# Kernel tuning notes

Hardware: AMD Instinct MI355X
Metric: run time of the kernel (lower is better)

## Reference

```python
import jax, jax.numpy as jnp
import numpy as np

N_NODES = 100000
NEG_SLOPE = 0.2  # PyG GATConv default LeakyReLU slope


def gat_conv(x, W, att_src, att_dst, bias, edge_index, num_nodes, concat):
    """PyG-style GATConv with default add_self_loops=True.
    x: [N, Fin], W: [Fin, H*C], att_src/att_dst: [H, C], bias: [H*C] or [C].
    """
    H, C = att_src.shape
    h = (x @ W).reshape(num_nodes, H, C)              # [N, H, C]
    # append self-loops (PyG default)
    loops = jnp.arange(num_nodes, dtype=edge_index.dtype)
    src = jnp.concatenate([edge_index[0], loops])     # [E+N]
    dst = jnp.concatenate([edge_index[1], loops])
    # per-node attention logits, then per-edge score
    a_src = jnp.sum(h * att_src[None], axis=-1)       # [N, H]
    a_dst = jnp.sum(h * att_dst[None], axis=-1)       # [N, H]
    e = jax.nn.leaky_relu(a_src[src] + a_dst[dst], NEG_SLOPE)  # [E+N, H]
    # softmax over incoming edges of each destination node
    m = jax.ops.segment_max(e, dst, num_segments=num_nodes)    # [N, H]
    e = jnp.exp(e - m[dst])
    denom = jax.ops.segment_sum(e, dst, num_segments=num_nodes)
    alpha = e / denom[dst]                                      # [E+N, H]
    # scatter-aggregate weighted source features
    msg = h[src] * alpha[..., None]                             # [E+N, H, C]
    out = jax.ops.segment_sum(msg, dst, num_segments=num_nodes)  # [N, H, C]
    if concat:
        out = out.reshape(num_nodes, H * C)
    else:
        out = out.mean(axis=1)
    return out + bias


def setup_inputs() -> dict:
    key = jax.random.key(0)
    ks = jax.random.split(key, 12)
    N, E = N_NODES, 1600000
    Fin, Ch, Hh, Cout = 128, 64, 2, 64

    def glorot(k, shape):
        fan = shape[0] + shape[-1]
        return jax.random.uniform(k, shape, jnp.float32, -1.0, 1.0) * np.sqrt(6.0 / fan)

    x = jax.random.normal(ks[0], (N, Fin), jnp.float32)
    edge_index = jax.random.randint(ks[1], (2, E), 0, N, jnp.int32)
    W1 = glorot(ks[2], (Fin, Hh * Ch))
    att_src1 = glorot(ks[3], (Hh, Ch))
    att_dst1 = glorot(ks[4], (Hh, Ch))
    b1 = jnp.zeros((Hh * Ch,), jnp.float32)
    W2 = glorot(ks[5], (Hh * Ch, Cout))
    att_src2 = glorot(ks[6], (1, Cout))
    att_dst2 = glorot(ks[7], (1, Cout))
    b2 = jnp.zeros((Cout,), jnp.float32)
    return {"x": x, "edge_index": edge_index,
            "W1": W1, "att_src1": att_src1, "att_dst1": att_dst1, "b1": b1,
            "W2": W2, "att_src2": att_src2, "att_dst2": att_dst2, "b2": b2}


def reference(x, edge_index, W1, att_src1, att_dst1, b1, W2, att_src2, att_dst2, b2):
    h = gat_conv(x, W1, att_src1, att_dst1, b1, edge_index, N_NODES, concat=True)
    h = jax.nn.elu(h)
    out = gat_conv(h, W2, att_src2, att_dst2, b2, edge_index, N_NODES, concat=True)
    return out
```

## Files before the change

kernel.cpp:

```cpp
#include <hip/hip_runtime.h>
#include <hip/hip_bf16.h>
#include <cstdint>
#include <cstddef>

static constexpr int FIN = 128;
static constexpr int HC1 = 128;
static constexpr int EPB = 4096;

typedef __attribute__((ext_vector_type(8))) short short8;
typedef __attribute__((ext_vector_type(4))) float f32x4;

__device__ __forceinline__ float bf2f(unsigned int u) { return __uint_as_float(u << 16); }
__device__ __forceinline__ unsigned short f2bf(float f) {
  unsigned int u = __float_as_uint(f);
  return (unsigned short)((u + 0x7fff + ((u >> 16) & 1)) >> 16);
}
__device__ __forceinline__ float lrelu02(float x) { return x > 0.f ? x : 0.2f * x; }
__device__ __forceinline__ int rl_i(int v, int l) { return __builtin_amdgcn_readlane(v, l); }
__device__ __forceinline__ unsigned int q8b(float x, float inv) {
  float q = fminf(fmaxf(x * inv, -127.f), 127.f);
  return (unsigned int)((int)rintf(q) + 128) & 255u;
}
#define NEG_INF __int_as_float(0xff800000)

__global__ __launch_bounds__(256) void bucket_hist(const int* __restrict__ dst,
                                                   int* __restrict__ bhist, int E, int NB) {
  __shared__ int lh[512];
  int t = threadIdx.x;
  lh[t] = 0; lh[t + 256] = 0;
  __syncthreads();
  int e0 = blockIdx.x * EPB;
  #pragma unroll
  for (int i = 0; i < EPB / 256; i++) {
    int e = e0 + i * 256 + t;
    if (e < E) atomicAdd(&lh[dst[e] >> 8], 1);
  }
  __syncthreads();
  for (int x = t; x < NB; x += 256) {
    int c = lh[x];
    if (c > 0) atomicAdd(&bhist[x], c);
  }
}

__global__ __launch_bounds__(512) void scan_buckets(const int* __restrict__ bhist,
                                                    int* __restrict__ boffs, int n) {
  __shared__ int sh[512];
  int t = threadIdx.x;
  int v = (t < n) ? bhist[t] : 0;
  sh[t] = v; __syncthreads();
  for (int d = 1; d < 512; d <<= 1) {
    int w = (t >= d) ? sh[t - d] : 0;
    __syncthreads();
    sh[t] += w;
    __syncthreads();
  }
  if (t <= n) boffs[t] = sh[t] - v;
}

__global__ __launch_bounds__(256) void bucket_scatter(const int* __restrict__ src,
                                                      const int* __restrict__ dst,
                                                      const int* __restrict__ boffs,
                                                      int* __restrict__ gcur,
                                                      unsigned int* __restrict__ sorted,
                                                      int E, int NB) {
  __shared__ int lh[512];
  int t = threadIdx.x;
  lh[t] = 0; lh[t + 256] = 0;
  __syncthreads();
  int e0 = blockIdx.x * EPB;
  #pragma unroll
  for (int i = 0; i < EPB / 256; i++) {
    int e = e0 + i * 256 + t;
    if (e < E) atomicAdd(&lh[dst[e] >> 8], 1);
  }
  __syncthreads();
  for (int x = t; x < NB; x += 256) {
    int c = lh[x];
    lh[x] = (c > 0) ? (boffs[x] + atomicAdd(&gcur[x], c)) : 0;
  }
  __syncthreads();
  #pragma unroll
  for (int i = 0; i < EPB / 256; i++) {
    int e = e0 + i * 256 + t;
    if (e < E) {
      int d = dst[e];
      int pos = atomicAdd(&lh[d >> 8], 1);
      sorted[pos] = ((unsigned int)src[e] << 8) | (unsigned int)(d & 255);
    }
  }
}

__global__ __launch_bounds__(256) void bucket_place_fused(const unsigned int* __restrict__ sorted,
                                                          const int* __restrict__ boffs,
                                                          int* __restrict__ offs,
                                                          int* __restrict__ ssrc,
                                                          int N, int E) {
  __shared__ int cnt[256];
  __shared__ int pref[256];
  int b = blockIdx.x, t = threadIdx.x;
  cnt[t] = 0;
  __syncthreads();
  int beg = boffs[b], end = boffs[b + 1];
  for (int p = beg + t; p < end; p += 256)
    atomicAdd(&cnt[sorted[p] & 255u], 1);
  __syncthreads();
  int v = cnt[t];
  pref[t] = v; __syncthreads();
  for (int d = 1; d < 256; d <<= 1) {
    int w = (t >= d) ? pref[t - d] : 0;
    __syncthreads();
    pref[t] += w;
    __syncthreads();
  }
  int excl = pref[t] - v;
  int node = b * 256 + t;
  if (node < N) offs[node] = beg + excl;
  if (b == 0 && t == 0) offs[N] = E;
  cnt[t] = beg + excl;
  __syncthreads();
  for (int p = beg + t; p < end; p += 256) {
    unsigned int pk = sorted[p];
    int dl = pk & 255u;
    int r = atomicAdd(&cnt[dl], 1);
    ssrc[r] = (int)(pk >> 8);
  }
}

template <int COLS, bool AF32>
__global__ __launch_bounds__(256) void gemm_mfma(const void* __restrict__ Av,
                                                 const float* __restrict__ Wv,
                                                 const float* __restrict__ att_s,
                                                 const float* __restrict__ att_d,
                                                 unsigned char* __restrict__ Cq,
                                                 float* __restrict__ scl,
                                                 float* __restrict__ asrc,
                                                 float* __restrict__ adst,
                                                 int nrows) {
  constexpr int NT = COLS / 16;
  constexpr int H = COLS / 64;
  __shared__ unsigned short WT[COLS][136];
  __shared__ __align__(16) unsigned char pack[4][16 * COLS];

  const int tid = threadIdx.x;
  constexpr int NPC = COLS / 4;
  for (int idx = tid; idx < 128 * NPC; idx += 256) {
    int k = idx / NPC;
    int n0 = (idx - k * NPC) * 4;
    float4 wv = *(const float4*)(Wv + (size_t)k * COLS + n0);
    WT[n0 + 0][k] = f2bf(wv.x);
    WT[n0 + 1][k] = f2bf(wv.y);
    WT[n0 + 2][k] = f2bf(wv.z);
    WT[n0 + 3][k] = f2bf(wv.w);
  }

  const int w = tid >> 6, lane = tid & 63;
  const int quad = lane >> 4, cl = lane & 15;
  const int rbase = blockIdx.x * 128 + w * 32;

  float asv[NT], adv[NT];
  #pragma unroll
  for (int ct = 0; ct < NT; ct++) {
    asv[ct] = att_s[ct * 16 + cl];
    adv[ct] = att_d[ct * 16 + cl];
  }
  __syncthreads();

  f32x4 acc[2][NT];
  #pragma unroll
  for (int rt = 0; rt < 2; rt++)
    #pragma unroll
    for (int ct = 0; ct < NT; ct++) acc[rt][ct] = (f32x4){0.f, 0.f, 0.f, 0.f};

  #pragma unroll
  for (int kc = 0; kc < 4; kc++) {
    const int k0 = kc * 32 + quad * 8;
    short8 a[2];
    #pragma unroll
    for (int rt = 0; rt < 2; rt++) {
      int row = rbase + rt * 16 + cl;
      row = min(row, nrows - 1);
      if constexpr (AF32) {
        const float* ap = (const float*)Av + (size_t)row * 128 + k0;
        float4 f0 = *(const float4*)ap;
        float4 f1 = *(const float4*)(ap + 4);
        short8 t;
        t[0] = (short)f2bf(f0.x); t[1] = (short)f2bf(f0.y);
        t[2] = (short)f2bf(f0.z); t[3] = (short)f2bf(f0.w);
        t[4] = (short)f2bf(f1.x); t[5] = (short)f2bf(f1.y);
        t[6] = (short)f2bf(f1.z); t[7] = (short)f2bf(f1.w);
        a[rt] = t;
      } else {
        a[rt] = *(const short8*)((const unsigned short*)Av + (size_t)row * 128 + k0);
      }
    }
    #pragma unroll
    for (int ct = 0; ct < NT; ct++) {
      short8 b = *(const short8*)&WT[ct * 16 + cl][k0];
      #pragma unroll
      for (int rt = 0; rt < 2; rt++)
        acc[rt][ct] = __builtin_amdgcn_mfma_f32_16x16x32_bf16(a[rt], b, acc[rt][ct], 0, 0, 0);
    }
  }

  #pragma unroll
  for (int rt = 0; rt < 2; rt++) {
    #pragma unroll
    for (int r = 0; r < 4; r++) {
      int grow = rbase + rt * 16 + quad * 4 + r;
      float s0 = 0.f, s1 = 0.f, d0 = 0.f, d1 = 0.f;
      float mx = 0.f;
      #pragma unroll
      for (int ct = 0; ct < NT; ct++) {
        float av = acc[rt][ct][r];
        mx = fmaxf(mx, fabsf(av));
        if (H == 2 && ct >= NT / 2) {
          s1 = fmaf(av, asv[ct], s1);
          d1 = fmaf(av, adv[ct], d1);
        } else {
          s0 = fmaf(av, asv[ct], s0);
          d0 = fmaf(av, adv[ct], d0);
        }
      }
      #pragma unroll
      for (int dd = 8; dd >= 1; dd >>= 1) {
        mx = fmaxf(mx, __shfl_xor(mx, dd));
        s0 += __shfl_xor(s0, dd);
        d0 += __shfl_xor(d0, dd);
        if (H == 2) {
          s1 += __shfl_xor(s1, dd);
          d1 += __shfl_xor(d1, dd);
        }
      }
      float inv = mx > 0.f ? 127.f / mx : 0.f;
      if (cl == 0 && grow < nrows) {
        scl[grow] = mx * (1.f / 127.f);
        if (H == 2) {
          ((float2*)asrc)[grow] = make_float2(s0, s1);
          ((float2*)adst)[grow] = make_float2(d0, d1);
        } else {
          asrc[grow] = s0;
          adst[grow] = d0;
        }
      }
      #pragma unroll
      for (int ct = 0; ct < NT; ct++)
        pack[w][(quad * 4 + r) * COLS + ct * 16 + cl] =
            (unsigned char)q8b(acc[rt][ct][r], inv);
    }
    __syncthreads();
    if constexpr (COLS == 128) {
      #pragma unroll
      for (int i = 0; i < 2; i++) {
        int off = i * 1024 + lane * 16;
        uint4 v = *(const uint4*)&pack[w][off];
        int grow = rbase + rt * 16 + (off >> 7);
        if (grow < nrows)
          *(uint4*)(Cq + (size_t)grow * 128 + (off & 127)) = v;
      }
    } else {
      int off = lane * 16;
      uint4 v = *(const uint4*)&pack[w][off];
      int grow = rbase + rt * 16 + (off >> 6);
      if (grow < nrows)
        *(uint4*)(Cq + (size_t)grow * 64 + (off & 63)) = v;
    }
    __syncthreads();
  }
}

template <int H, bool ELU_OUT, bool F32OUT>
__global__ __launch_bounds__(256) void agg_gather(const void* __restrict__ hq,
                                                  const float* __restrict__ scl,
                                                  const float* __restrict__ asrc,
                                                  const float* __restrict__ adst,
                                                  const int* __restrict__ offs,
                                                  const int* __restrict__ ssrc,
                                                  const float* __restrict__ bias,
                                                  void* __restrict__ outv, int n) {
  __shared__ float pshare[4][64];
  __shared__ int vshare[4][64];
  const int tid = threadIdx.x;
  const int wid = tid >> 6;
  int node = (int)((blockIdx.x * (unsigned)blockDim.x + tid) >> 6);
  int lane = tid & 63;
  if (node >= n) return;
  const int hd = lane >> 5;
  const int beg = offs[node], end = offs[node + 1];
  const unsigned short* hq16 = (const unsigned short*)hq;
  const unsigned char* hqb = (const unsigned char*)hq;

  float adh, p_self, acc0, acc1;
  const float s_self = scl[node];
  if constexpr (H == 2) {
    float2 adv = ((const float2*)adst)[node];
    float2 asv = ((const float2*)asrc)[node];
    adh = hd ? adv.y : adv.x;
    p_self = __expf(lrelu02((hd ? asv.y : asv.x) + adh));
    unsigned int v = hq16[((size_t)node << 6) + lane];
    float ps = p_self * s_self;
    acc0 = ps * ((float)(v & 255u) - 128.f);
    acc1 = ps * ((float)((v >> 8) & 255u) - 128.f);
  } else {
    adh = adst[node];
    p_self = __expf(lrelu02(asrc[node] + adh));
    if (hd == 0) {
      unsigned int v = hq16[((size_t)node << 5) + lane];
      float ps = p_self * s_self;
      acc0 = ps * ((float)(v & 255u) - 128.f);
      acc1 = ps * ((float)((v >> 8) & 255u) - 128.f);
    } else {
      acc0 = 0.f; acc1 = 0.f;
    }
  }
  float dacc = 0.f;
  float SPF = 0.f;

  constexpr int CH = (H == 2) ? 32 : 64;
  const int lvoff = (lane & 31) * 2;
  for (int pos = beg; pos < end; pos += CH) {
    const int len = min(CH, end - pos);
    int li = (H == 2) ? (lane & 31) : lane;
    bool valid = li < len;
    int s_l = valid ? ssrc[pos + li] : 0;
    float scl_l = valid ? scl[s_l] : 0.f;
    float a;
    if constexpr (H == 2) a = asrc[(s_l << 1) + hd];
    else                  a = asrc[s_l];
    float e_l = lrelu02(a + adh);
    float p_l = valid ? __expf(e_l) : 0.f;
    dacc += p_l;
    p_l *= scl_l;
    SPF += p_l;
    pshare[wid][lane] = p_l;
    if constexpr (H == 1) vshare[wid][lane] = s_l << 6;

    if constexpr (H == 2) {
      const int ng = (len + 7) >> 3;
      for (int g = 0; g < ng; g++) {
        const int jb = g * 8;
        unsigned short v[8];
        #pragma unroll
        for (int k = 0; k < 8; k++) {
          int s = rl_i(s_l, jb + k);
          v[k] = hq16[((size_t)(unsigned)s << 6) + lane];
        }
        float pv[8];
        #pragma unroll
        for (int k = 0; k < 8; k++) pv[k] = pshare[wid][hd * 32 + jb + k];
        #pragma unroll
        for (int k = 0; k < 8; k++) {
          unsigned int w = v[k];
          acc0 = fmaf(pv[k], (float)(w & 255u), acc0);
          acc1 = fmaf(pv[k], (float)((w >> 8) & 255u), acc1);
        }
      }
    } else {
      const int npair = (len + 1) >> 1;
      const int ng = (npair + 7) >> 3;
      for (int g = 0; g < ng; g++) {
        const int jb = g * 16;
        unsigned short v[8];
        #pragma unroll
        for (int k = 0; k < 8; k++) {
          int voff = vshare[wid][jb + 2 * k + hd];
          v[k] = *(const unsigned short*)(hqb + (unsigned)voff + lvoff);
        }
        float pv[8];
        #pragma unroll
        for (int k = 0; k < 8; k++) pv[k] = pshare[wid][jb + 2 * k + hd];
        #pragma unroll
        for (int k = 0; k < 8; k++) {
          unsigned int w = v[k];
          acc0 = fmaf(pv[k], (float)(w & 255u), acc0);
          acc1 = fmaf(pv[k], (float)((w >> 8) & 255u), acc1);
        }
      }
    }
  }

  if constexpr (H == 2) {
    #pragma unroll
    for (int dlt = 16; dlt >= 1; dlt >>= 1) {
      dacc += __shfl_xor(dacc, dlt);
      SPF  += __shfl_xor(SPF, dlt);
    }
  } else {
    #pragma unroll
    for (int dlt = 32; dlt >= 1; dlt >>= 1) {
      dacc += __shfl_xor(dacc, dlt);
      SPF  += __shfl_xor(SPF, dlt);
    }
    acc0 += __shfl_xor(acc0, 32);
    acc1 += __shfl_xor(acc1, 32);
  }
  acc0 = fmaf(-128.f, SPF, acc0);
  acc1 = fmaf(-128.f, SPF, acc1);
  const float d = p_self + dacc;

  const float inv = 1.f / d;
  if constexpr (H == 2) {
    float2 bv = ((const float2*)bias)[lane];
    float v0 = acc0 * inv + bv.x;
    float v1 = acc1 * inv + bv.y;
    if (ELU_OUT) {
      v0 = v0 > 0.f ? v0 : (__expf(v0) - 1.f);
      v1 = v1 > 0.f ? v1 : (__expf(v1) - 1.f);
    }
    if constexpr (F32OUT) {
      ((float2*)outv)[(size_t)node * 64 + lane] = make_float2(v0, v1);
    } else {
      unsigned int pk = (unsigned int)f2bf(v0) | ((unsigned int)f2bf(v1) << 16);
      ((unsigned int*)outv)[(size_t)node * 64 + lane] = pk;
    }
  } else {
    if (hd == 0) {
      float2 bv = ((const float2*)bias)[lane];
      float v0 = acc0 * inv + bv.x;
      float v1 = acc1 * inv + bv.y;
      if (ELU_OUT) {
        v0 = v0 > 0.f ? v0 : (__expf(v0) - 1.f);
        v1 = v1 > 0.f ? v1 : (__expf(v1) - 1.f);
      }
      if constexpr (F32OUT) {
        ((float2*)outv)[(size_t)node * 32 + lane] = make_float2(v0, v1);
      } else {
        unsigned int pk = (unsigned int)f2bf(v0) | ((unsigned int)f2bf(v1) << 16);
        ((unsigned int*)outv)[(size_t)node * 32 + lane] = pk;
      }
    }
  }
}

extern "C" void kernel_launch(void* const* d_in, const int* in_sizes, int n_in,
                              void* d_out, int out_size, void* d_ws, size_t ws_size,
                              hipStream_t stream) {
  const int N = in_sizes[0] / FIN;
  const int E = in_sizes[1] / 2;

  const void*  x   = d_in[0];
  const int*   ei  = (const int*)d_in[1];
  const float* W1  = (const float*)d_in[2];
  const float* as1 = (const float*)d_in[3];
  const float* ad1 = (const float*)d_in[4];
  const float* b1  = (const float*)d_in[5];
  const float* W2  = (const float*)d_in[6];
  const float* as2 = (const float*)d_in[7];
  const float* ad2 = (const float*)d_in[8];
  const float* b2  = (const float*)d_in[9];

  const int* e_src = ei;
  const int* e_dst = ei + E;

  char* p = (char*)d_ws;
  auto carve = [&](size_t bytes) {
    char* q = p;
    p += (bytes + 255) & ~(size_t)255;
    return (void*)q;
  };
  unsigned char* h1q = (unsigned char*)carve((size_t)N * 128);
  float* scl1        = (float*)carve((size_t)N * 4);
  unsigned char* h2q = (unsigned char*)carve((size_t)N * 64);
  float* scl2        = (float*)carve((size_t)N * 4);
  unsigned short* buf2 = (unsigned short*)carve((size_t)N * HC1 * 2);
  float* asrc1 = (float*)carve((size_t)N * 2 * 4);
  float* adst1 = (float*)carve((size_t)N * 2 * 4);
  float* asrc2 = (float*)carve((size_t)N * 4);
  float* adst2 = (float*)carve((size_t)N * 4);
  int* offs    = (int*)carve((size_t)(N + 1) * 4);
  int* bhist   = (int*)carve((size_t)2 * 512 * 4);
  int* gcur    = bhist + 512;
  int* boffs   = (int*)carve(513 * 4);
  unsigned int* sorted = (unsigned int*)carve((size_t)E * 4);
  int* ssrc    = (int*)carve((size_t)E * 4);

  const int NB = (N + 255) >> 8;
  const int sgrid = (E + EPB - 1) / EPB;
  const int wgrid = (int)(((size_t)N * 64 + 255) / 256);
  const int ggrid = (N + 127) / 128;

  hipMemsetAsync(bhist, 0, (size_t)2 * 512 * 4, stream);
  bucket_hist<<<sgrid, 256, 0, stream>>>(e_dst, bhist, E, NB);
  scan_buckets<<<1, 512, 0, stream>>>(bhist, boffs, NB);
  bucket_scatter<<<sgrid, 256, 0, stream>>>(e_src, e_dst, boffs, gcur, sorted, E, NB);
  bucket_place_fused<<<NB, 256, 0, stream>>>(sorted, boffs, offs, ssrc, N, E);

  gemm_mfma<128, true><<<ggrid, 256, 0, stream>>>(x, W1, as1, ad1, h1q, scl1,
                                                  asrc1, adst1, N);
  agg_gather<2, true, false><<<wgrid, 256, 0, stream>>>(h1q, scl1, asrc1, adst1,
                                                        offs, ssrc, b1, buf2, N);

  gemm_mfma<64, false><<<ggrid, 256, 0, stream>>>(buf2, W2, as2, ad2, h2q, scl2,
                                                  asrc2, adst2, N);
  agg_gather<1, false, true><<<wgrid, 256, 0, stream>>>(h2q, scl2, asrc2, adst2,
                                                        offs, ssrc, b2, d_out, N);
}
```

Before: 306.3 us.

## Store node features as fp16 and aggregate with packed fdot2 online softmax

Replaces the per-row int8 quantized node features (with per-node scale) with fp16 storage, doubling the gather bytes per edge but removing the scale loads and dequantization arithmetic. The aggregation switches to an online max-subtracted softmax and uses packed fp16 probabilities with v_dot2 instructions to accumulate two edges per instruction. It trades memory traffic in the gather-heavy aggregation for fewer ALU ops and better numerical accuracy.

```diff
diff --git a/kernel.cpp b/kernel.cpp
--- a/kernel.cpp
+++ b/kernel.cpp
@@ -9,17 +9,22 @@
 
 typedef __attribute__((ext_vector_type(8))) short short8;
 typedef __attribute__((ext_vector_type(4))) float f32x4;
-
-__device__ __forceinline__ float bf2f(unsigned int u) { return __uint_as_float(u << 16); }
+typedef __attribute__((ext_vector_type(2))) _Float16 f16x2;
+typedef decltype(__builtin_amdgcn_cvt_pkrtz(0.f, 0.f)) pk16x2;
+
 __device__ __forceinline__ unsigned short f2bf(float f) {
   unsigned int u = __float_as_uint(f);
   return (unsigned short)((u + 0x7fff + ((u >> 16) & 1)) >> 16);
 }
+__device__ __forceinline__ unsigned short f2h(float f) {
+  union { _Float16 h; unsigned short u; } c; c.h = (_Float16)f; return c.u;
+}
 __device__ __forceinline__ float lrelu02(float x) { return x > 0.f ? x : 0.2f * x; }
 __device__ __forceinline__ int rl_i(int v, int l) { return __builtin_amdgcn_readlane(v, l); }
-__device__ __forceinline__ unsigned int q8b(float x, float inv) {
-  float q = fminf(fmaxf(x * inv, -127.f), 127.f);
-  return (unsigned int)((int)rintf(q) + 128) & 255u;
+__device__ __forceinline__ float fdot2u(unsigned int a, unsigned int b, float c) {
+  union { unsigned int u; f16x2 h; } ua, ub;
+  ua.u = a; ub.u = b;
+  return __builtin_amdgcn_fdot2(ua.h, ub.h, c, false);
 }
 #define NEG_INF __int_as_float(0xff800000)
 
@@ -132,14 +137,13 @@
                                                  const float* __restrict__ att_s,
                                                  const float* __restrict__ att_d,
                                                  unsigned char* __restrict__ Cq,
-                                                 float* __restrict__ scl,
                                                  float* __restrict__ asrc,
                                                  float* __restrict__ adst,
                                                  int nrows) {
   constexpr int NT = COLS / 16;
   constexpr int H = COLS / 64;
   __shared__ unsigned short WT[COLS][136];
-  __shared__ __align__(16) unsigned char pack[4][16 * COLS];
+  __shared__ __align__(16) unsigned short pack16[4][16 * COLS];
 
   const int tid = threadIdx.x;
   constexpr int NPC = COLS / 4;
@@ -208,11 +212,9 @@
     for (int r = 0; r < 4; r++) {
       int grow = rbase + rt * 16 + quad * 4 + r;
       float s0 = 0.f, s1 = 0.f, d0 = 0.f, d1 = 0.f;
-      float mx = 0.f;
       #pragma unroll
       for (int ct = 0; ct < NT; ct++) {
         float av = acc[rt][ct][r];
-        mx = fmaxf(mx, fabsf(av));
         if (H == 2 && ct >= NT / 2) {
           s1 = fmaf(av, asv[ct], s1);
           d1 = fmaf(av, adv[ct], d1);
@@ -223,7 +225,6 @@
       }
       #pragma unroll
       for (int dd = 8; dd >= 1; dd >>= 1) {
-        mx = fmaxf(mx, __shfl_xor(mx, dd));
         s0 += __shfl_xor(s0, dd);
         d0 += __shfl_xor(d0, dd);
         if (H == 2) {
@@ -231,9 +232,7 @@
           d1 += __shfl_xor(d1, dd);
         }
       }
-      float inv = mx > 0.f ? 127.f / mx : 0.f;
       if (cl == 0 && grow < nrows) {
-        scl[grow] = mx * (1.f / 127.f);
         if (H == 2) {
           ((float2*)asrc)[grow] = make_float2(s0, s1);
           ((float2*)adst)[grow] = make_float2(d0, d1);
@@ -244,25 +243,27 @@
       }
       #pragma unroll
       for (int ct = 0; ct < NT; ct++)
-        pack[w][(quad * 4 + r) * COLS + ct * 16 + cl] =
-            (unsigned char)q8b(acc[rt][ct][r], inv);
+        pack16[w][(quad * 4 + r) * COLS + ct * 16 + cl] = f2h(acc[rt][ct][r]);
     }
     __syncthreads();
     if constexpr (COLS == 128) {
+      #pragma unroll
+      for (int i = 0; i < 4; i++) {
+        int off = i * 1024 + lane * 16;
+        uint4 v = *(const uint4*)((const char*)pack16[w] + off);
+        int grow = rbase + rt * 16 + (off >> 8);
+        if (grow < nrows)
+          *(uint4*)(Cq + (size_t)grow * 256 + (off & 255)) = v;
+      }
+    } else {
       #pragma unroll
       for (int i = 0; i < 2; i++) {
         int off = i * 1024 + lane * 16;
-        uint4 v = *(const uint4*)&pack[w][off];
+        uint4 v = *(const uint4*)((const char*)pack16[w] + off);
         int grow = rbase + rt * 16 + (off >> 7);
         if (grow < nrows)
           *(uint4*)(Cq + (size_t)grow * 128 + (off & 127)) = v;
       }
-    } else {
-      int off = lane * 16;
-      uint4 v = *(const uint4*)&pack[w][off];
-      int grow = rbase + rt * 16 + (off >> 6);
-      if (grow < nrows)
-        *(uint4*)(Cq + (size_t)grow * 64 + (off & 63)) = v;
     }
     __syncthreads();
   }
@@ -270,15 +271,13 @@
 
 template <int H, bool ELU_OUT, bool F32OUT>
 __global__ __launch_bounds__(256) void agg_gather(const void* __restrict__ hq,
-                                                  const float* __restrict__ scl,
                                                   const float* __restrict__ asrc,
                                                   const float* __restrict__ adst,
                                                   const int* __restrict__ offs,
                                                   const int* __restrict__ ssrc,
                                                   const float* __restrict__ bias,
                                                   void* __restrict__ outv, int n) {
-  __shared__ float pshare[4][64];
-  __shared__ int vshare[4][64];
+  __shared__ unsigned int pshare[4][32];
   const int tid = threadIdx.x;
   const int wid = tid >> 6;
   int node = (int)((blockIdx.x * (unsigned)blockDim.x + tid) >> 6);
@@ -286,118 +285,103 @@
   if (node >= n) return;
   const int hd = lane >> 5;
   const int beg = offs[node], end = offs[node + 1];
+  const unsigned int* hq32 = (const unsigned int*)hq;
   const unsigned short* hq16 = (const unsigned short*)hq;
-  const unsigned char* hqb = (const unsigned char*)hq;
-
-  float adh, p_self, acc0, acc1;
-  const float s_self = scl[node];
+
+  float adh, m, acc0, acc1;
   if constexpr (H == 2) {
     float2 adv = ((const float2*)adst)[node];
     float2 asv = ((const float2*)asrc)[node];
     adh = hd ? adv.y : adv.x;
-    p_self = __expf(lrelu02((hd ? asv.y : asv.x) + adh));
-    unsigned int v = hq16[((size_t)node << 6) + lane];
-    float ps = p_self * s_self;
-    acc0 = ps * ((float)(v & 255u) - 128.f);
-    acc1 = ps * ((float)((v >> 8) & 255u) - 128.f);
+    m = lrelu02((hd ? asv.y : asv.x) + adh);
+    union { unsigned int u; f16x2 h; } c;
+    c.u = hq32[((size_t)node << 6) + lane];
+    acc0 = (float)c.h[0];
+    acc1 = (float)c.h[1];
   } else {
     adh = adst[node];
-    p_self = __expf(lrelu02(asrc[node] + adh));
-    if (hd == 0) {
-      unsigned int v = hq16[((size_t)node << 5) + lane];
-      float ps = p_self * s_self;
-      acc0 = ps * ((float)(v & 255u) - 128.f);
-      acc1 = ps * ((float)((v >> 8) & 255u) - 128.f);
-    } else {
-      acc0 = 0.f; acc1 = 0.f;
-    }
-  }
+    m = lrelu02(asrc[node] + adh);
+    union { unsigned short u; _Float16 h; } c;
+    c.u = hq16[((size_t)node << 6) + lane];
+    acc0 = (float)c.h;
+    acc1 = 0.f;
+  }
+  float dsf = 1.f;
   float dacc = 0.f;
-  float SPF = 0.f;
 
   constexpr int CH = (H == 2) ? 32 : 64;
-  const int lvoff = (lane & 31) * 2;
   for (int pos = beg; pos < end; pos += CH) {
     const int len = min(CH, end - pos);
     int li = (H == 2) ? (lane & 31) : lane;
     bool valid = li < len;
     int s_l = valid ? ssrc[pos + li] : 0;
-    float scl_l = valid ? scl[s_l] : 0.f;
     float a;
     if constexpr (H == 2) a = asrc[(s_l << 1) + hd];
     else                  a = asrc[s_l];
-    float e_l = lrelu02(a + adh);
-    float p_l = valid ? __expf(e_l) : 0.f;
-    dacc += p_l;
-    p_l *= scl_l;
-    SPF += p_l;
-    pshare[wid][lane] = p_l;
-    if constexpr (H == 1) vshare[wid][lane] = s_l << 6;
+    float e_l = valid ? lrelu02(a + adh) : NEG_INF;
+    float mc = e_l;
+    #pragma unroll
+    for (int dlt = CH >> 1; dlt >= 1; dlt >>= 1) mc = fmaxf(mc, __shfl_xor(mc, dlt));
+    float m_new = fmaxf(m, mc);
+    float f = __expf(m - m_new);
+    float p_l = __expf(e_l - m_new);
+    dacc = fmaf(dacc, f, p_l);
+    acc0 *= f; acc1 *= f; dsf *= f;
+    m = m_new;
+    float po = __shfl_xor(p_l, 1);
+    float plo = (li & 1) ? po : p_l;
+    float phi = (li & 1) ? p_l : po;
+    union { pk16x2 h; unsigned int u; } pc;
+    pc.h = __builtin_amdgcn_cvt_pkrtz(plo, phi);
+    pshare[wid][((H == 2) ? (hd << 4) : 0) + (li >> 1)] = pc.u;
 
     if constexpr (H == 2) {
       const int ng = (len + 7) >> 3;
       for (int g = 0; g < ng; g++) {
         const int jb = g * 8;
-        unsigned short v[8];
+        uint4 pp = *(const uint4*)&pshare[wid][(hd << 4) + (jb >> 1)];
+        unsigned int ppa[4] = {pp.x, pp.y, pp.z, pp.w};
+        #pragma unroll
+        for (int k = 0; k < 4; k++) {
+          int s0 = rl_i(s_l, jb + 2 * k);
+          int s1 = rl_i(s_l, jb + 2 * k + 1);
+          unsigned int v0 = hq32[((size_t)(unsigned)s0 << 6) + lane];
+          unsigned int v1 = hq32[((size_t)(unsigned)s1 << 6) + lane];
+          unsigned int lo = __builtin_amdgcn_perm(v1, v0, 0x05040100u);
+          unsigned int hi = __builtin_amdgcn_perm(v1, v0, 0x07060302u);
+          acc0 = fdot2u(ppa[k], lo, acc0);
+          acc1 = fdot2u(ppa[k], hi, acc1);
+        }
+      }
+    } else {
+      const int ng = (len + 15) >> 4;
+      for (int g = 0; g < ng; g++) {
+        const int jb = g * 16;
+        uint4 ppx = *(const uint4*)&pshare[wid][(jb >> 1)];
+        uint4 ppy = *(const uint4*)&pshare[wid][(jb >> 1) + 4];
+        unsigned int ppa[8] = {ppx.x, ppx.y, ppx.z, ppx.w, ppy.x, ppy.y, ppy.z, ppy.w};
         #pragma unroll
         for (int k = 0; k < 8; k++) {
-          int s = rl_i(s_l, jb + k);
-          v[k] = hq16[((size_t)(unsigned)s << 6) + lane];
+          int s0 = rl_i(s_l, jb + 2 * k);
+          int s1 = rl_i(s_l, jb + 2 * k + 1);
+          unsigned int v0 = hq16[((size_t)(unsigned)s0 << 6) + lane];
+          unsigned int v1 = hq16[((size_t)(unsigned)s1 << 6) + lane];
+          unsigned int mg = __builtin_amdgcn_perm(v1, v0, 0x05040100u);
+          acc0 = fdot2u(ppa[k], mg, acc0);
         }
-        float pv[8];
-        #pragma unroll
-        for (int k = 0; k < 8; k++) pv[k] = pshare[wid][hd * 32 + jb + k];
-        #pragma unroll
-        for (int k = 0; k < 8; k++) {
-          unsigned int w = v[k];
-          acc0 = fmaf(pv[k], (float)(w & 255u), acc0);
-          acc1 = fmaf(pv[k], (float)((w >> 8) & 255u), acc1);
-        }
-      }
-    } else {
-      const int npair = (len + 1) >> 1;
-      const int ng = (npair + 7) >> 3;
-      for (int g = 0; g < ng; g++) {
-        const int jb = g * 16;
-        unsigned short v[8];
-        #pragma unroll
-        for (int k = 0; k < 8; k++) {
-          int voff = vshare[wid][jb + 2 * k + hd];
-          v[k] = *(const unsigned short*)(hqb + (unsigned)voff + lvoff);
-        }
-        float pv[8];
-        #pragma unroll
-        for (int k = 0; k < 8; k++) pv[k] = pshare[wid][jb + 2 * k + hd];
-        #pragma unroll
-        for (int k = 0; k < 8; k++) {
-          unsigned int w = v[k];
-          acc0 = fmaf(pv[k], (float)(w & 255u), acc0);
-          acc1 = fmaf(pv[k], (float)((w >> 8) & 255u), acc1);
-        }
       }
     }
   }
 
   if constexpr (H == 2) {
     #pragma unroll
-    for (int dlt = 16; dlt >= 1; dlt >>= 1) {
-      dacc += __shfl_xor(dacc, dlt);
-      SPF  += __shfl_xor(SPF, dlt);
-    }
+    for (int dlt = 16; dlt >= 1; dlt >>= 1) dacc += __shfl_xor(dacc, dlt);
   } else {
     #pragma unroll
-    for (int dlt = 32; dlt >= 1; dlt >>= 1) {
-      dacc += __shfl_xor(dacc, dlt);
-      SPF  += __shfl_xor(SPF, dlt);
-    }
-    acc0 += __shfl_xor(acc0, 32);
-    acc1 += __shfl_xor(acc1, 32);
-  }
-  acc0 = fmaf(-128.f, SPF, acc0);
-  acc1 = fmaf(-128.f, SPF, acc1);
-  const float d = p_self + dacc;
-
-  const float inv = 1.f / d;
+    for (int dlt = 32; dlt >= 1; dlt >>= 1) dacc += __shfl_xor(dacc, dlt);
+  }
+  const float inv = 1.f / (dsf + dacc);
+
   if constexpr (H == 2) {
     float2 bv = ((const float2*)bias)[lane];
     float v0 = acc0 * inv + bv.x;
@@ -413,20 +397,12 @@
       ((unsigned int*)outv)[(size_t)node * 64 + lane] = pk;
     }
   } else {
-    if (hd == 0) {
-      float2 bv = ((const float2*)bias)[lane];
-      float v0 = acc0 * inv + bv.x;
-      float v1 = acc1 * inv + bv.y;
-      if (ELU_OUT) {
-        v0 = v0 > 0.f ? v0 : (__expf(v0) - 1.f);
-        v1 = v1 > 0.f ? v1 : (__expf(v1) - 1.f);
-      }
-      if constexpr (F32OUT) {
-        ((float2*)outv)[(size_t)node * 32 + lane] = make_float2(v0, v1);
-      } else {
-        unsigned int pk = (unsigned int)f2bf(v0) | ((unsigned int)f2bf(v1) << 16);
-        ((unsigned int*)outv)[(size_t)node * 32 + lane] = pk;
-      }
+    float v0 = acc0 * inv + bias[lane];
+    if (ELU_OUT) v0 = v0 > 0.f ? v0 : (__expf(v0) - 1.f);
+    if constexpr (F32OUT) {
+      ((float*)outv)[(size_t)node * 64 + lane] = v0;
+    } else {
+      ((unsigned short*)outv)[(size_t)node * 64 + lane] = f2bf(v0);
     }
   }
 }
@@ -457,10 +433,8 @@
     p += (bytes + 255) & ~(size_t)255;
     return (void*)q;
   };
-  unsigned char* h1q = (unsigned char*)carve((size_t)N * 128);
-  float* scl1        = (float*)carve((size_t)N * 4);
-  unsigned char* h2q = (unsigned char*)carve((size_t)N * 64);
-  float* scl2        = (float*)carve((size_t)N * 4);
+  unsigned char* h1f = (unsigned char*)carve((size_t)N * 256);
+  unsigned char* h2f = (unsigned char*)carve((size_t)N * 128);
   unsigned short* buf2 = (unsigned short*)carve((size_t)N * HC1 * 2);
   float* asrc1 = (float*)carve((size_t)N * 2 * 4);
   float* adst1 = (float*)carve((size_t)N * 2 * 4);
@@ -484,13 +458,13 @@
   bucket_scatter<<<sgrid, 256, 0, stream>>>(e_src, e_dst, boffs, gcur, sorted, E, NB);
   bucket_place_fused<<<NB, 256, 0, stream>>>(sorted, boffs, offs, ssrc, N, E);
 
-  gemm_mfma<128, true><<<ggrid, 256, 0, stream>>>(x, W1, as1, ad1, h1q, scl1,
+  gemm_mfma<128, true><<<ggrid, 256, 0, stream>>>(x, W1, as1, ad1, h1f,
                                                   asrc1, adst1, N);
-  agg_gather<2, true, false><<<wgrid, 256, 0, stream>>>(h1q, scl1, asrc1, adst1,
+  agg_gather<2, true, false><<<wgrid, 256, 0, stream>>>(h1f, asrc1, adst1,
                                                         offs, ssrc, b1, buf2, N);
 
-  gemm_mfma<64, false><<<ggrid, 256, 0, stream>>>(buf2, W2, as2, ad2, h2q, scl2,
+  gemm_mfma<64, false><<<ggrid, 256, 0, stream>>>(buf2, W2, as2, ad2, h2f,
                                                   asrc2, adst2, N);
-  agg_gather<1, false, true><<<wgrid, 256, 0, stream>>>(h2q, scl2, asrc2, adst2,
+  agg_gather<1, false, true><<<wgrid, 256, 0, stream>>>(h2f, asrc2, adst2,
                                                         offs, ssrc, b2, d_out, N);
 }
```

New measurement: 319.3 us. 4.3% more time.

## Fold attention vectors into weights and compute logits via extra MFMA tile

Applied to the files above, without the earlier changes.

Precomputes u = W·att_src and W·att_dst in a small kernel. Those vectors, split into bf16 high and low parts, are appended as an extra 16-column tile of the GEMM B operand, so the attention logits come out of one more MFMA per k-chunk. This replaces the per-row FMA dot products and the cross-lane shuffle reductions that followed the GEMM. It also halves the aggregation block size to 128 threads, changing occupancy and scheduling granularity. The cost is extra MFMA work, a little more LDS, and a small precision change in the logits from the bf16 hi/lo split.

```diff
diff --git a/kernel.cpp b/kernel.cpp
--- a/kernel.cpp
+++ b/kernel.cpp
@@ -126,11 +126,40 @@
   }
 }
 
+__global__ __launch_bounds__(128) void att_fold(const float* __restrict__ W1,
+                                                const float* __restrict__ as1,
+                                                const float* __restrict__ ad1,
+                                                const float* __restrict__ W2,
+                                                const float* __restrict__ as2,
+                                                const float* __restrict__ ad2,
+                                                float* __restrict__ u1,
+                                                float* __restrict__ u2) {
+  int t = threadIdx.x;
+  if (blockIdx.x == 0) {
+    float s0 = 0.f, s1 = 0.f, d0 = 0.f, d1 = 0.f;
+    for (int c = 0; c < 64; c++) {
+      float w0 = W1[t * 128 + c], w1 = W1[t * 128 + 64 + c];
+      s0 = fmaf(w0, as1[c], s0);
+      s1 = fmaf(w1, as1[64 + c], s1);
+      d0 = fmaf(w0, ad1[c], d0);
+      d1 = fmaf(w1, ad1[64 + c], d1);
+    }
+    u1[t] = s0; u1[128 + t] = s1; u1[256 + t] = d0; u1[384 + t] = d1;
+  } else {
+    float s = 0.f, d = 0.f;
+    for (int c = 0; c < 64; c++) {
+      float w = W2[t * 64 + c];
+      s = fmaf(w, as2[c], s);
+      d = fmaf(w, ad2[c], d);
+    }
+    u2[t] = s; u2[128 + t] = d;
+  }
+}
+
 template <int COLS, bool AF32>
 __global__ __launch_bounds__(256) void gemm_mfma(const void* __restrict__ Av,
                                                  const float* __restrict__ Wv,
-                                                 const float* __restrict__ att_s,
-                                                 const float* __restrict__ att_d,
+                                                 const float* __restrict__ uvec,
                                                  unsigned char* __restrict__ Cq,
                                                  float* __restrict__ scl,
                                                  float* __restrict__ asrc,
@@ -138,7 +167,8 @@
                                                  int nrows) {
   constexpr int NT = COLS / 16;
   constexpr int H = COLS / 64;
-  __shared__ unsigned short WT[COLS][136];
+  constexpr int NU = (H == 2) ? 4 : 2;
+  __shared__ unsigned short WT[COLS + 16][136];
   __shared__ __align__(16) unsigned char pack[4][16 * COLS];
 
   const int tid = threadIdx.x;
@@ -152,24 +182,29 @@
     WT[n0 + 2][k] = f2bf(wv.z);
     WT[n0 + 3][k] = f2bf(wv.w);
   }
+  for (int idx = tid; idx < 16 * 128; idx += 256) {
+    int c = idx >> 7;
+    int k = idx & 127;
+    unsigned short val = 0;
+    if (c < NU) {
+      val = f2bf(uvec[c * 128 + k]);
+    } else if (c >= 4 && c < 4 + NU) {
+      float u = uvec[(c - 4) * 128 + k];
+      val = f2bf(u - bf2f(f2bf(u)));
+    }
+    WT[COLS + c][k] = val;
+  }
 
   const int w = tid >> 6, lane = tid & 63;
   const int quad = lane >> 4, cl = lane & 15;
   const int rbase = blockIdx.x * 128 + w * 32;
-
-  float asv[NT], adv[NT];
-  #pragma unroll
-  for (int ct = 0; ct < NT; ct++) {
-    asv[ct] = att_s[ct * 16 + cl];
-    adv[ct] = att_d[ct * 16 + cl];
-  }
-  __syncthreads();
-
-  f32x4 acc[2][NT];
+  __syncthreads();
+
+  f32x4 acc[2][NT + 1];
   #pragma unroll
   for (int rt = 0; rt < 2; rt++)
     #pragma unroll
-    for (int ct = 0; ct < NT; ct++) acc[rt][ct] = (f32x4){0.f, 0.f, 0.f, 0.f};
+    for (int ct = 0; ct <= NT; ct++) acc[rt][ct] = (f32x4){0.f, 0.f, 0.f, 0.f};
 
   #pragma unroll
   for (int kc = 0; kc < 4; kc++) {
@@ -194,7 +229,7 @@
       }
     }
     #pragma unroll
-    for (int ct = 0; ct < NT; ct++) {
+    for (int ct = 0; ct <= NT; ct++) {
       short8 b = *(const short8*)&WT[ct * 16 + cl][k0];
       #pragma unroll
       for (int rt = 0; rt < 2; rt++)
@@ -207,41 +242,24 @@
     #pragma unroll
     for (int r = 0; r < 4; r++) {
       int grow = rbase + rt * 16 + quad * 4 + r;
-      float s0 = 0.f, s1 = 0.f, d0 = 0.f, d1 = 0.f;
       float mx = 0.f;
       #pragma unroll
-      for (int ct = 0; ct < NT; ct++) {
-        float av = acc[rt][ct][r];
-        mx = fmaxf(mx, fabsf(av));
-        if (H == 2 && ct >= NT / 2) {
-          s1 = fmaf(av, asv[ct], s1);
-          d1 = fmaf(av, adv[ct], d1);
+      for (int ct = 0; ct < NT; ct++) mx = fmaxf(mx, fabsf(acc[rt][ct][r]));
+      #pragma unroll
+      for (int dd = 8; dd >= 1; dd >>= 1) mx = fmaxf(mx, __shfl_xor(mx, dd));
+      float av = acc[rt][NT][r];
+      av += __shfl_xor(av, 4);
+      if (grow < nrows) {
+        if (cl == 0) scl[grow] = mx * (1.f / 127.f);
+        if constexpr (H == 2) {
+          if (cl < 2) asrc[grow * 2 + cl] = av;
+          else if (cl < 4) adst[grow * 2 + (cl - 2)] = av;
         } else {
-          s0 = fmaf(av, asv[ct], s0);
-          d0 = fmaf(av, adv[ct], d0);
+          if (cl == 0) asrc[grow] = av;
+          else if (cl == 1) adst[grow] = av;
         }
       }
-      #pragma unroll
-      for (int dd = 8; dd >= 1; dd >>= 1) {
-        mx = fmaxf(mx, __shfl_xor(mx, dd));
-        s0 += __shfl_xor(s0, dd);
-        d0 += __shfl_xor(d0, dd);
-        if (H == 2) {
-          s1 += __shfl_xor(s1, dd);
-          d1 += __shfl_xor(d1, dd);
-        }
-      }
       float inv = mx > 0.f ? 127.f / mx : 0.f;
-      if (cl == 0 && grow < nrows) {
-        scl[grow] = mx * (1.f / 127.f);
-        if (H == 2) {
-          ((float2*)asrc)[grow] = make_float2(s0, s1);
-          ((float2*)adst)[grow] = make_float2(d0, d1);
-        } else {
-          asrc[grow] = s0;
-          adst[grow] = d0;
-        }
-      }
       #pragma unroll
       for (int ct = 0; ct < NT; ct++)
         pack[w][(quad * 4 + r) * COLS + ct * 16 + cl] =
@@ -269,7 +287,7 @@
 }
 
 template <int H, bool ELU_OUT, bool F32OUT>
-__global__ __launch_bounds__(256) void agg_gather(const void* __restrict__ hq,
+__global__ __launch_bounds__(128) void agg_gather(const void* __restrict__ hq,
                                                   const float* __restrict__ scl,
                                                   const float* __restrict__ asrc,
                                                   const float* __restrict__ adst,
@@ -277,8 +295,8 @@
                                                   const int* __restrict__ ssrc,
                                                   const float* __restrict__ bias,
                                                   void* __restrict__ outv, int n) {
-  __shared__ float pshare[4][64];
-  __shared__ int vshare[4][64];
+  __shared__ float pshare[2][64];
+  __shared__ int vshare[2][64];
   const int tid = threadIdx.x;
   const int wid = tid >> 6;
   int node = (int)((blockIdx.x * (unsigned)blockDim.x + tid) >> 6);
@@ -466,6 +484,8 @@
   float* adst1 = (float*)carve((size_t)N * 2 * 4);
   float* asrc2 = (float*)carve((size_t)N * 4);
   float* adst2 = (float*)carve((size_t)N * 4);
+  float* u1    = (float*)carve(4 * 128 * 4);
+  float* u2    = (float*)carve(2 * 128 * 4);
   int* offs    = (int*)carve((size_t)(N + 1) * 4);
   int* bhist   = (int*)carve((size_t)2 * 512 * 4);
   int* gcur    = bhist + 512;
@@ -475,22 +495,23 @@
 
   const int NB = (N + 255) >> 8;
   const int sgrid = (E + EPB - 1) / EPB;
-  const int wgrid = (int)(((size_t)N * 64 + 255) / 256);
+  const int wgrid = (int)(((size_t)N * 64 + 127) / 128);
   const int ggrid = (N + 127) / 128;
 
   hipMemsetAsync(bhist, 0, (size_t)2 * 512 * 4, stream);
+  att_fold<<<2, 128, 0, stream>>>(W1, as1, ad1, W2, as2, ad2, u1, u2);
   bucket_hist<<<sgrid, 256, 0, stream>>>(e_dst, bhist, E, NB);
   scan_buckets<<<1, 512, 0, stream>>>(bhist, boffs, NB);
   bucket_scatter<<<sgrid, 256, 0, stream>>>(e_src, e_dst, boffs, gcur, sorted, E, NB);
   bucket_place_fused<<<NB, 256, 0, stream>>>(sorted, boffs, offs, ssrc, N, E);
 
-  gemm_mfma<128, true><<<ggrid, 256, 0, stream>>>(x, W1, as1, ad1, h1q, scl1,
+  gemm_mfma<128, true><<<ggrid, 256, 0, stream>>>(x, W1, u1, h1q, scl1,
                                                   asrc1, adst1, N);
-  agg_gather<2, true, false><<<wgrid, 256, 0, stream>>>(h1q, scl1, asrc1, adst1,
+  agg_gather<2, true, false><<<wgrid, 128, 0, stream>>>(h1q, scl1, asrc1, adst1,
                                                         offs, ssrc, b1, buf2, N);
 
-  gemm_mfma<64, false><<<ggrid, 256, 0, stream>>>(buf2, W2, as2, ad2, h2q, scl2,
+  gemm_mfma<64, false><<<ggrid, 256, 0, stream>>>(buf2, W2, u2, h2q, scl2,
                                                   asrc2, adst2, N);
-  agg_gather<1, false, true><<<wgrid, 256, 0, stream>>>(h2q, scl2, asrc2, adst2,
+  agg_gather<1, false, true><<<wgrid, 128, 0, stream>>>(h2q, scl2, asrc2, adst2,
                                                         offs, ssrc, b2, d_out, N);
 }
```

Measured after the change: 307.0 us. About the same (+0.2%).
